# Kernel optimization log

Measured on AMD Instinct MI355X. Metric: run time of the kernel, lower is better.

## Reference

```python
import jax, jax.numpy as jnp
import numpy as np

N, F, T, HID, E = 50000, 8, 12, 64, 1600000


def setup_inputs() -> dict:
    key = jax.random.key(0)
    ks = jax.random.split(key, 9)
    x = jax.random.normal(ks[0], (N, F, T), jnp.float32)
    edge_index = jax.random.randint(ks[1], (2, E), 0, N)
    edge_weight = jax.random.uniform(ks[2], (E,), jnp.float32)
    # GCNConv weights for the z/r/h gates, fused along the output dim -> (F, 3*HID)
    s = 1.0 / np.sqrt(F)
    conv_w = jax.random.uniform(ks[3], (F, 3 * HID), jnp.float32, -s, s)
    conv_b = jnp.zeros((3 * HID,), jnp.float32)
    # TGCN gate linears: input is concat([conv_out, H]) of width 2*HID
    s2 = 1.0 / np.sqrt(2 * HID)
    lin_w = jax.random.uniform(ks[4], (3, 2 * HID, HID), jnp.float32, -s2, s2)
    lin_b = jax.random.uniform(ks[5], (3, HID), jnp.float32, -s2, s2)
    attention = jax.random.uniform(ks[6], (T,), jnp.float32)
    sc = 1.0 / np.sqrt(HID)
    cls_w = jax.random.uniform(ks[7], (HID, T), jnp.float32, -sc, sc)
    cls_b = jax.random.uniform(ks[8], (T,), jnp.float32, -sc, sc)
    return dict(x=x, edge_index=edge_index, edge_weight=edge_weight,
                conv_w=conv_w, conv_b=conv_b, lin_w=lin_w, lin_b=lin_b,
                attention=attention, cls_w=cls_w, cls_b=cls_b)


def _gcn_norm(edge_index, edge_weight, num_nodes):
    # PyG gcn_norm: add self-loops (weight 1), symmetric D^-1/2 (A+I) D^-1/2
    src, dst = edge_index[0], edge_index[1]
    loop = jnp.arange(num_nodes)
    src = jnp.concatenate([src, loop])
    dst = jnp.concatenate([dst, loop])
    w = jnp.concatenate([edge_weight, jnp.ones((num_nodes,), edge_weight.dtype)])
    deg = jax.ops.segment_sum(w, dst, num_segments=num_nodes)
    dinv = jnp.where(deg > 0, jax.lax.rsqrt(deg), 0.0)
    return src, dst, dinv[src] * w * dinv[dst]


def reference(x, edge_index, edge_weight, conv_w, conv_b, lin_w, lin_b, attention, cls_w, cls_b):
    num_nodes, _, periods = x.shape
    hid = cls_w.shape[0]
    src, dst, norm = _gcn_norm(edge_index, edge_weight, num_nodes)
    probs = jax.nn.softmax(attention)
    Hzero = jnp.zeros((num_nodes, hid), x.dtype)  # A3TGCN passes the same H (None->0) each period
    H_accum = jnp.zeros((num_nodes, hid), x.dtype)
    for t in range(periods):
        xw = x[:, :, t] @ conv_w  # (N, 3*hid)
        conv = jax.ops.segment_sum(xw[src] * norm[:, None], dst, num_segments=num_nodes) + conv_b
        cz, cr, ch = jnp.split(conv, 3, axis=1)
        Z = jax.nn.sigmoid(jnp.concatenate([cz, Hzero], axis=1) @ lin_w[0] + lin_b[0])
        R = jax.nn.sigmoid(jnp.concatenate([cr, Hzero], axis=1) @ lin_w[1] + lin_b[1])
        H_tilde = jnp.tanh(jnp.concatenate([ch, Hzero * R], axis=1) @ lin_w[2] + lin_b[2])
        H_new = Z * Hzero + (1.0 - Z) * H_tilde
        H_accum = H_accum + probs[t] * H_new
    h = jax.nn.relu(H_accum)
    return h @ cls_w + cls_b  # (N, periods)
```

## Files before the change

kernel.cpp:

```cpp
#include <hip/hip_runtime.h>
#include <hip/hip_fp16.h>
#include <math.h>

#define NN 50000
#define FD 8
#define TD 12
#define HD 64
#define FT 96
#define EE 1600000
#define NBUK 391
#define TILE 16384
#define NT 98
#define SORTCAP 5120

#define OFF_GHIST 0
#define OFF_BASE  512
#define OFF_CUR   1024
#define OFF_ROWST 2048
#define OFF_DINV  (2048 + NN + 16)
#define OFF_FUSED (OFF_DINV + NN)
#define OFF_XH    (OFF_FUSED + 1184)
#define OFF_BEDGE (OFF_XH + NN*48)
#define OFF_AGGH  (OFF_BEDGE + 2*EE)

__device__ inline void h8f(uint4 h, float* f) {
    const __half2* p = (const __half2*)&h;
#pragma unroll
    for (int i = 0; i < 4; ++i) {
        float2 v = __half22float2(p[i]);
        f[2 * i] = v.x; f[2 * i + 1] = v.y;
    }
}

__device__ inline uint4 f8h(const float* f) {
    uint4 o;
    __half2* p = (__half2*)&o;
#pragma unroll
    for (int i = 0; i < 4; ++i) p[i] = __floats2half2_rn(f[2 * i], f[2 * i + 1]);
    return o;
}

__global__ void k_precompute(const float* __restrict__ conv_w,
                             const float* __restrict__ conv_b,
                             const float* __restrict__ lin_w,
                             const float* __restrict__ lin_b,
                             const float* __restrict__ attention,
                             float* __restrict__ fused,
                             int* __restrict__ ghist) {
    int tid = threadIdx.x;
    if (tid < NBUK) ghist[tid] = 0;
    for (int idx = tid; idx < 1024; idx += blockDim.x) {
        int sel = idx >> 9;
        int f = (idx & 511) >> 6;
        int h = idx & 63;
        const float* cw = conv_w + f * 192 + (sel ? 128 : 0);
        const float* lw = lin_w + (sel ? 2 * 128 * 64 : 0) + h;
        float s = 0.f;
        for (int k = 0; k < 64; ++k) s += cw[k] * lw[k * 64];
        fused[idx] = s;
    }
    for (int idx = tid; idx < 128; idx += blockDim.x) {
        int sel = idx >> 6;
        int h = idx & 63;
        const float* cb = conv_b + (sel ? 128 : 0);
        const float* lw = lin_w + (sel ? 2 * 128 * 64 : 0) + h;
        float s = lin_b[(sel ? 2 * 64 : 0) + h];
        for (int k = 0; k < 64; ++k) s += cb[k] * lw[k * 64];
        fused[1024 + idx] = s;
    }
    if (tid == 0) {
        float m = attention[0];
        for (int t = 1; t < TD; ++t) m = fmaxf(m, attention[t]);
        float e[TD], sum = 0.f;
        for (int t = 0; t < TD; ++t) { e[t] = __expf(attention[t] - m); sum += e[t]; }
        for (int t = 0; t < TD; ++t) fused[1152 + t] = e[t] / sum;
    }
}

__global__ void k_xhalf(const float* __restrict__ x, uint4* __restrict__ xh4) {
    unsigned i = blockIdx.x * 256u + threadIdx.x;
    if (i >= (unsigned)NN * 12u) return;
    unsigned n = i / 12u, t = i - n * 12u;
    const float* xp = x + (size_t)n * FT + t;
    float f[8];
#pragma unroll
    for (int k = 0; k < 8; ++k) f[k] = xp[k * 12];
    xh4[i] = f8h(f);
}

__global__ __launch_bounds__(1024) void k_hist(const int* __restrict__ ei,
                                               int* __restrict__ ghist) {
    __shared__ int h[NBUK];
    int tid = threadIdx.x;
    for (int i = tid; i < NBUK; i += 1024) h[i] = 0;
    __syncthreads();
    int base = blockIdx.x * TILE;
    for (int i = 0; i < TILE / 1024; ++i) {
        int e = base + i * 1024 + tid;
        if (e < EE) atomicAdd(&h[ei[EE + e] >> 7], 1);
    }
    __syncthreads();
    for (int i = tid; i < NBUK; i += 1024)
        if (h[i]) atomicAdd(&ghist[i], h[i]);
}

__global__ void k_scan(const int* __restrict__ ghist, int* __restrict__ bktbase,
                       int* __restrict__ cursor) {
    __shared__ int s[512];
    int tid = threadIdx.x;
    int v = (tid < NBUK) ? ghist[tid] : 0;
    s[tid] = v;
    __syncthreads();
    for (int off = 1; off < 512; off <<= 1) {
        int t = (tid >= off) ? s[tid - off] : 0;
        __syncthreads();
        s[tid] += t;
        __syncthreads();
    }
    int excl = s[tid] - v;
    if (tid < NBUK) { bktbase[tid] = excl; cursor[tid] = excl; }
    if (tid == NBUK - 1) bktbase[NBUK] = excl + v;
}

__global__ __launch_bounds__(1024) void k_place(const int* __restrict__ ei,
                                                const float* __restrict__ w,
                                                int* __restrict__ cursor,
                                                int2* __restrict__ bedge) {
    __shared__ int h[NBUK], bbase[NBUK];
    int tid = threadIdx.x;
    for (int i = tid; i < NBUK; i += 1024) h[i] = 0;
    __syncthreads();
    int base = blockIdx.x * TILE;
    for (int i = 0; i < TILE / 1024; ++i) {
        int e = base + i * 1024 + tid;
        if (e < EE) atomicAdd(&h[ei[EE + e] >> 7], 1);
    }
    __syncthreads();
    for (int i = tid; i < NBUK; i += 1024) {
        int c = h[i];
        bbase[i] = c ? atomicAdd(&cursor[i], c) : 0;
        h[i] = 0;
    }
    __syncthreads();
    for (int i = 0; i < TILE / 1024; ++i) {
        int e = base + i * 1024 + tid;
        if (e < EE) {
            int dst = ei[EE + e];
            int bk = dst >> 7;
            int rank = atomicAdd(&h[bk], 1);
            bedge[bbase[bk] + rank] =
                make_int2(ei[e] | ((dst & 127) << 16), __float_as_int(w[e]));
        }
    }
}

__global__ __launch_bounds__(512) void k_sort(const int* __restrict__ bktbase,
                                              int2* __restrict__ bedge,
                                              int* __restrict__ rowstart,
                                              float* __restrict__ dinv) {
    __shared__ int2 stage[SORTCAP];
    __shared__ int cnt[128];
    __shared__ float wd[128];
    __shared__ int rowbase[128];
    int tid = threadIdx.x, b = blockIdx.x;
    int es = bktbase[b], ee = bktbase[b + 1];
    int count = ee - es;
    if (count > SORTCAP) count = SORTCAP;
    if (tid < 128) { cnt[tid] = 0; wd[tid] = 0.f; }
    __syncthreads();
    for (int i = tid; i < count; i += 512) {
        int2 u = bedge[es + i];
        stage[i] = u;
        int dl = u.x >> 16;
        atomicAdd(&cnt[dl], 1);
        atomicAdd(&wd[dl], __int_as_float(u.y));
    }
    __syncthreads();
    if (tid < 128) rowbase[tid] = cnt[tid];
    __syncthreads();
    for (int off = 1; off < 128; off <<= 1) {
        int t = 0;
        if (tid >= off && tid < 128) t = rowbase[tid - off];
        __syncthreads();
        if (tid < 128) rowbase[tid] += t;
        __syncthreads();
    }
    int dbase = b << 7;
    if (tid < 128) {
        int excl = rowbase[tid] - cnt[tid];
        rowbase[tid] = excl;
        if (dbase + tid < NN) {
            rowstart[dbase + tid] = es + excl;
            dinv[dbase + tid] = rsqrtf(1.0f + wd[tid]);
        }
        cnt[tid] = 0;
    }
    if (b == NBUK - 1 && tid == 0) rowstart[NN] = ee;
    __syncthreads();
    for (int i = tid; i < count; i += 512) {
        int2 u = stage[i];
        int dl = u.x >> 16;
        int pos = atomicAdd(&cnt[dl], 1);
        bedge[es + rowbase[dl] + pos] = make_int2(u.x & 0xFFFF, u.y);
    }
}

__global__ __launch_bounds__(256) void k_gather(const uint4* __restrict__ xh4,
                                                const float* __restrict__ dinv,
                                                const int* __restrict__ rowstart,
                                                const int2* __restrict__ edata,
                                                uint4* __restrict__ aggh) {
    unsigned t = blockIdx.x * 256u + threadIdx.x;
    if (t >= (unsigned)NN * 12u) return;
    unsigned n = t / 12u;
    unsigned c = t - n * 12u;
    float dv = dinv[n];
    float a[8];
    h8f(xh4[n * 12u + c], a);
#pragma unroll
    for (int j = 0; j < 8; ++j) a[j] *= dv;
    int rs = rowstart[n], re = rowstart[n + 1];
    int k = rs;
    for (; k + 1 < re; k += 2) {
        int2 pa = edata[k], pb = edata[k + 1];
        float ca = dinv[pa.x] * __int_as_float(pa.y);
        float cb = dinv[pb.x] * __int_as_float(pb.y);
        float va[8], vb[8];
        h8f(xh4[(unsigned)pa.x * 12u + c], va);
        h8f(xh4[(unsigned)pb.x * 12u + c], vb);
#pragma unroll
        for (int j = 0; j < 8; ++j) a[j] += ca * va[j] + cb * vb[j];
    }
    if (k < re) {
        int2 p = edata[k];
        float co = dinv[p.x] * __int_as_float(p.y);
        float v[8];
        h8f(xh4[(unsigned)p.x * 12u + c], v);
#pragma unroll
        for (int j = 0; j < 8; ++j) a[j] += co * v[j];
    }
#pragma unroll
    for (int j = 0; j < 8; ++j) a[j] *= dv;
    aggh[n * 12u + c] = f8h(a);
}

__global__ __launch_bounds__(256) void k_node(const uint4* __restrict__ aggh,
                                              const float* __restrict__ fused,
                                              const float* __restrict__ cls_w,
                                              const float* __restrict__ cls_b,
                                              float* __restrict__ out) {
    __shared__ float r_lds[32 * 100];
    __shared__ float rel_lds[32 * 68];
    __shared__ float cwT_lds[12 * 68];
    __shared__ float cb_lds[12];
    __shared__ float probs_lds[12];
    int tid = threadIdx.x;
    int nbase = blockIdx.x * 32;

    for (int id = tid; id < 384; id += 256) {
        int nl = id / 12, c = id - nl * 12;
        float f[8] = {0, 0, 0, 0, 0, 0, 0, 0};
        int n = nbase + nl;
        if (n < NN) h8f(aggh[(size_t)n * 12 + c], f);
        *(float4*)&r_lds[nl * 100 + c * 8] = make_float4(f[0], f[1], f[2], f[3]);
        *(float4*)&r_lds[nl * 100 + c * 8 + 4] = make_float4(f[4], f[5], f[6], f[7]);
    }
    for (int id = tid; id < 768; id += 256) {
        int hh = id / 12, t = id - hh * 12;
        cwT_lds[t * 68 + hh] = cls_w[id];
    }
    if (tid < 12) { cb_lds[tid] = cls_b[tid]; probs_lds[tid] = fused[1152 + tid]; }

    int h = tid & 63;
    int w = tid >> 6;
    float wz[FD], wh[FD];
#pragma unroll
    for (int f = 0; f < FD; ++f) {
        wz[f] = fused[f * 64 + h];
        wh[f] = fused[512 + f * 64 + h];
    }
    float bz = fused[1024 + h], bh = fused[1088 + h];
    __syncthreads();

#pragma unroll
    for (int np = 0; np < 4; ++np) {
        int nl0 = w * 8 + np * 2;
        const float* rp0 = &r_lds[nl0 * 100];
        const float* rp1 = rp0 + 100;
        float acc0 = 0.f, acc1 = 0.f;
#pragma unroll
        for (int t = 0; t < TD; ++t) {
            float4 a0 = *(const float4*)&rp0[t * 8];
            float4 a1 = *(const float4*)&rp0[t * 8 + 4];
            float4 b0 = *(const float4*)&rp1[t * 8];
            float4 b1 = *(const float4*)&rp1[t * 8 + 4];
            float z0 = bz, h0 = bh, z1 = bz, h1 = bh;
            z0 += a0.x * wz[0] + a0.y * wz[1] + a0.z * wz[2] + a0.w * wz[3]
                + a1.x * wz[4] + a1.y * wz[5] + a1.z * wz[6] + a1.w * wz[7];
            h0 += a0.x * wh[0] + a0.y * wh[1] + a0.z * wh[2] + a0.w * wh[3]
                + a1.x * wh[4] + a1.y * wh[5] + a1.z * wh[6] + a1.w * wh[7];
            z1 += b0.x * wz[0] + b0.y * wz[1] + b0.z * wz[2] + b0.w * wz[3]
                + b1.x * wz[4] + b1.y * wz[5] + b1.z * wz[6] + b1.w * wz[7];
            h1 += b0.x * wh[0] + b0.y * wh[1] + b0.z * wh[2] + b0.w * wh[3]
                + b1.x * wh[4] + b1.y * wh[5] + b1.z * wh[6] + b1.w * wh[7];
            float om0 = __builtin_amdgcn_rcpf(1.f + __expf(z0));
            float om1 = __builtin_amdgcn_rcpf(1.f + __expf(z1));
            float Ht0 = 1.f - 2.f * __builtin_amdgcn_rcpf(1.f + __expf(2.f * h0));
            float Ht1 = 1.f - 2.f * __builtin_amdgcn_rcpf(1.f + __expf(2.f * h1));
            float p = probs_lds[t];
            acc0 += p * om0 * Ht0;
            acc1 += p * om1 * Ht1;
        }
        rel_lds[nl0 * 68 + h] = fmaxf(acc0, 0.f);
        rel_lds[(nl0 + 1) * 68 + h] = fmaxf(acc1, 0.f);
    }
    __syncthreads();

    for (int id = tid; id < 384; id += 256) {
        int nl = id / 12, t = id - nl * 12;
        int n = nbase + nl;
        if (n >= NN) continue;
        const float* rl = &rel_lds[nl * 68];
        const float* cwr = &cwT_lds[t * 68];
        float s = cb_lds[t];
#pragma unroll
        for (int k = 0; k < 16; ++k) {
            float4 rv = *(const float4*)&rl[k * 4];
            float4 cv = *(const float4*)&cwr[k * 4];
            s += rv.x * cv.x + rv.y * cv.y + rv.z * cv.z + rv.w * cv.w;
        }
        out[(size_t)n * TD + t] = s;
    }
}

extern "C" void kernel_launch(void* const* d_in, const int* in_sizes, int n_in,
                              void* d_out, int out_size, void* d_ws, size_t ws_size,
                              hipStream_t stream) {
    const float* x         = (const float*)d_in[0];
    const int*   ei        = (const int*)d_in[1];
    const float* w         = (const float*)d_in[2];
    const float* conv_w    = (const float*)d_in[3];
    const float* conv_b    = (const float*)d_in[4];
    const float* lin_w     = (const float*)d_in[5];
    const float* lin_b     = (const float*)d_in[6];
    const float* attention = (const float*)d_in[7];
    const float* cls_w     = (const float*)d_in[8];
    const float* cls_b     = (const float*)d_in[9];
    float* ws  = (float*)d_ws;
    float* out = (float*)d_out;

    int*   ghist    = (int*)(ws + OFF_GHIST);
    int*   bktbase  = (int*)(ws + OFF_BASE);
    int*   cursor   = (int*)(ws + OFF_CUR);
    int*   rowstart = (int*)(ws + OFF_ROWST);
    float* dinv     = ws + OFF_DINV;
    float* fused    = ws + OFF_FUSED;
    uint4* xh4      = (uint4*)(ws + OFF_XH);
    int2*  bedge    = (int2*)(ws + OFF_BEDGE);
    uint4* aggh     = (uint4*)(ws + OFF_AGGH);

    k_precompute<<<1, 512, 0, stream>>>(conv_w, conv_b, lin_w, lin_b, attention,
                                        fused, ghist);
    k_xhalf<<<(NN * 12 + 255) / 256, 256, 0, stream>>>(x, xh4);
    k_hist<<<NT, 1024, 0, stream>>>(ei, ghist);
    k_scan<<<1, 512, 0, stream>>>(ghist, bktbase, cursor);
    k_place<<<NT, 1024, 0, stream>>>(ei, w, cursor, bedge);
    k_sort<<<NBUK, 512, 0, stream>>>(bktbase, bedge, rowstart, dinv);
    {
        unsigned total = (unsigned)NN * 12u;
        k_gather<<<(total + 255) / 256, 256, 0, stream>>>(xh4, dinv,
                                                          rowstart, bedge, aggh);
    }
    k_node<<<(NN + 31) / 32, 256, 0, stream>>>(aggh, fused, cls_w, cls_b, out);
}
```

Before: 166.8 us.

## Fuse front kernels, reuse per-tile histograms in place, unroll gather by four

Merges the precompute, x-to-half conversion and edge histogram kernels into one launch that partitions its blocks by role, with the ghist clear moved to a memset. Each histogram tile now writes its per-bucket counts to a workspace array, so the place kernel no longer re-reads destinations and recounts them. The gather inner loop is unrolled from two to four edges to keep more loads in flight. The cost is extra workspace, a memset launch, and higher register pressure in the gather kernel.

```diff
diff --git a/kernel.cpp b/kernel.cpp
--- a/kernel.cpp
+++ b/kernel.cpp
@@ -11,6 +11,7 @@
 #define NBUK 391
 #define TILE 16384
 #define NT 98
+#define XB 586
 #define SORTCAP 5120
 
 #define OFF_GHIST 0
@@ -19,7 +20,8 @@
 #define OFF_ROWST 2048
 #define OFF_DINV  (2048 + NN + 16)
 #define OFF_FUSED (OFF_DINV + NN)
-#define OFF_XH    (OFF_FUSED + 1184)
+#define OFF_THIST (OFF_FUSED + 1184)
+#define OFF_XH    (OFF_THIST + 38400)
 #define OFF_BEDGE (OFF_XH + NN*48)
 #define OFF_AGGH  (OFF_BEDGE + 2*EE)
 
@@ -40,68 +42,73 @@
     return o;
 }
 
-__global__ void k_precompute(const float* __restrict__ conv_w,
-                             const float* __restrict__ conv_b,
-                             const float* __restrict__ lin_w,
-                             const float* __restrict__ lin_b,
-                             const float* __restrict__ attention,
-                             float* __restrict__ fused,
-                             int* __restrict__ ghist) {
+__global__ __launch_bounds__(1024) void k_front(const float* __restrict__ x,
+                                                uint4* __restrict__ xh4,
+                                                const int* __restrict__ ei,
+                                                int* __restrict__ ghist,
+                                                int* __restrict__ thist,
+                                                const float* __restrict__ conv_w,
+                                                const float* __restrict__ conv_b,
+                                                const float* __restrict__ lin_w,
+                                                const float* __restrict__ lin_b,
+                                                const float* __restrict__ attention,
+                                                float* __restrict__ fused) {
+    int b = blockIdx.x;
     int tid = threadIdx.x;
-    if (tid < NBUK) ghist[tid] = 0;
-    for (int idx = tid; idx < 1024; idx += blockDim.x) {
-        int sel = idx >> 9;
-        int f = (idx & 511) >> 6;
-        int h = idx & 63;
-        const float* cw = conv_w + f * 192 + (sel ? 128 : 0);
-        const float* lw = lin_w + (sel ? 2 * 128 * 64 : 0) + h;
-        float s = 0.f;
-        for (int k = 0; k < 64; ++k) s += cw[k] * lw[k * 64];
-        fused[idx] = s;
-    }
-    for (int idx = tid; idx < 128; idx += blockDim.x) {
-        int sel = idx >> 6;
-        int h = idx & 63;
-        const float* cb = conv_b + (sel ? 128 : 0);
-        const float* lw = lin_w + (sel ? 2 * 128 * 64 : 0) + h;
-        float s = lin_b[(sel ? 2 * 64 : 0) + h];
-        for (int k = 0; k < 64; ++k) s += cb[k] * lw[k * 64];
-        fused[1024 + idx] = s;
-    }
-    if (tid == 0) {
-        float m = attention[0];
-        for (int t = 1; t < TD; ++t) m = fmaxf(m, attention[t]);
-        float e[TD], sum = 0.f;
-        for (int t = 0; t < TD; ++t) { e[t] = __expf(attention[t] - m); sum += e[t]; }
-        for (int t = 0; t < TD; ++t) fused[1152 + t] = e[t] / sum;
-    }
-}
-
-__global__ void k_xhalf(const float* __restrict__ x, uint4* __restrict__ xh4) {
-    unsigned i = blockIdx.x * 256u + threadIdx.x;
-    if (i >= (unsigned)NN * 12u) return;
-    unsigned n = i / 12u, t = i - n * 12u;
-    const float* xp = x + (size_t)n * FT + t;
-    float f[8];
-#pragma unroll
-    for (int k = 0; k < 8; ++k) f[k] = xp[k * 12];
-    xh4[i] = f8h(f);
-}
-
-__global__ __launch_bounds__(1024) void k_hist(const int* __restrict__ ei,
-                                               int* __restrict__ ghist) {
-    __shared__ int h[NBUK];
-    int tid = threadIdx.x;
-    for (int i = tid; i < NBUK; i += 1024) h[i] = 0;
-    __syncthreads();
-    int base = blockIdx.x * TILE;
-    for (int i = 0; i < TILE / 1024; ++i) {
-        int e = base + i * 1024 + tid;
-        if (e < EE) atomicAdd(&h[ei[EE + e] >> 7], 1);
-    }
-    __syncthreads();
-    for (int i = tid; i < NBUK; i += 1024)
-        if (h[i]) atomicAdd(&ghist[i], h[i]);
+    if (b < NT) {
+        __shared__ int h[NBUK];
+        for (int i = tid; i < NBUK; i += 1024) h[i] = 0;
+        __syncthreads();
+        int base = b * TILE;
+        for (int i = 0; i < TILE / 1024; ++i) {
+            int e = base + i * 1024 + tid;
+            if (e < EE) atomicAdd(&h[ei[EE + e] >> 7], 1);
+        }
+        __syncthreads();
+        int* trow = thist + b * NBUK;
+        for (int i = tid; i < NBUK; i += 1024) {
+            int c = h[i];
+            trow[i] = c;
+            if (c) atomicAdd(&ghist[i], c);
+        }
+    } else if (b < NT + XB) {
+        unsigned i = (unsigned)(b - NT) * 1024u + tid;
+        if (i < (unsigned)NN * 12u) {
+            unsigned n = i / 12u, t = i - n * 12u;
+            const float* xp = x + (size_t)n * FT + t;
+            float f[8];
+#pragma unroll
+            for (int k = 0; k < 8; ++k) f[k] = xp[k * 12];
+            xh4[i] = f8h(f);
+        }
+    } else {
+        for (int idx = tid; idx < 1024; idx += 1024) {
+            int sel = idx >> 9;
+            int f = (idx & 511) >> 6;
+            int h = idx & 63;
+            const float* cw = conv_w + f * 192 + (sel ? 128 : 0);
+            const float* lw = lin_w + (sel ? 2 * 128 * 64 : 0) + h;
+            float s = 0.f;
+            for (int k = 0; k < 64; ++k) s += cw[k] * lw[k * 64];
+            fused[idx] = s;
+        }
+        if (tid < 128) {
+            int sel = tid >> 6;
+            int h = tid & 63;
+            const float* cb = conv_b + (sel ? 128 : 0);
+            const float* lw = lin_w + (sel ? 2 * 128 * 64 : 0) + h;
+            float s = lin_b[(sel ? 2 * 64 : 0) + h];
+            for (int k = 0; k < 64; ++k) s += cb[k] * lw[k * 64];
+            fused[1024 + tid] = s;
+        }
+        if (tid == 0) {
+            float m = attention[0];
+            for (int t = 1; t < TD; ++t) m = fmaxf(m, attention[t]);
+            float e[TD], sum = 0.f;
+            for (int t = 0; t < TD; ++t) { e[t] = __expf(attention[t] - m); sum += e[t]; }
+            for (int t = 0; t < TD; ++t) fused[1152 + t] = e[t] / sum;
+        }
+    }
 }
 
 __global__ void k_scan(const int* __restrict__ ghist, int* __restrict__ bktbase,
@@ -124,24 +131,19 @@
 
 __global__ __launch_bounds__(1024) void k_place(const int* __restrict__ ei,
                                                 const float* __restrict__ w,
+                                                const int* __restrict__ thist,
                                                 int* __restrict__ cursor,
                                                 int2* __restrict__ bedge) {
     __shared__ int h[NBUK], bbase[NBUK];
     int tid = threadIdx.x;
-    for (int i = tid; i < NBUK; i += 1024) h[i] = 0;
-    __syncthreads();
-    int base = blockIdx.x * TILE;
-    for (int i = 0; i < TILE / 1024; ++i) {
-        int e = base + i * 1024 + tid;
-        if (e < EE) atomicAdd(&h[ei[EE + e] >> 7], 1);
-    }
-    __syncthreads();
+    const int* tcnt = thist + blockIdx.x * NBUK;
     for (int i = tid; i < NBUK; i += 1024) {
-        int c = h[i];
+        int c = tcnt[i];
         bbase[i] = c ? atomicAdd(&cursor[i], c) : 0;
         h[i] = 0;
     }
     __syncthreads();
+    int base = blockIdx.x * TILE;
     for (int i = 0; i < TILE / 1024; ++i) {
         int e = base + i * 1024 + tid;
         if (e < EE) {
@@ -221,17 +223,22 @@
     for (int j = 0; j < 8; ++j) a[j] *= dv;
     int rs = rowstart[n], re = rowstart[n + 1];
     int k = rs;
-    for (; k + 1 < re; k += 2) {
-        int2 pa = edata[k], pb = edata[k + 1];
-        float ca = dinv[pa.x] * __int_as_float(pa.y);
-        float cb = dinv[pb.x] * __int_as_float(pb.y);
-        float va[8], vb[8];
-        h8f(xh4[(unsigned)pa.x * 12u + c], va);
-        h8f(xh4[(unsigned)pb.x * 12u + c], vb);
-#pragma unroll
-        for (int j = 0; j < 8; ++j) a[j] += ca * va[j] + cb * vb[j];
-    }
-    if (k < re) {
+    for (; k + 3 < re; k += 4) {
+        int2 p0 = edata[k], p1 = edata[k + 1], p2 = edata[k + 2], p3 = edata[k + 3];
+        float c0 = dinv[p0.x] * __int_as_float(p0.y);
+        float c1 = dinv[p1.x] * __int_as_float(p1.y);
+        float c2 = dinv[p2.x] * __int_as_float(p2.y);
+        float c3 = dinv[p3.x] * __int_as_float(p3.y);
+        float v0[8], v1[8], v2[8], v3[8];
+        h8f(xh4[(unsigned)p0.x * 12u + c], v0);
+        h8f(xh4[(unsigned)p1.x * 12u + c], v1);
+        h8f(xh4[(unsigned)p2.x * 12u + c], v2);
+        h8f(xh4[(unsigned)p3.x * 12u + c], v3);
+#pragma unroll
+        for (int j = 0; j < 8; ++j)
+            a[j] += c0 * v0[j] + c1 * v1[j] + c2 * v2[j] + c3 * v3[j];
+    }
+    for (; k < re; ++k) {
         int2 p = edata[k];
         float co = dinv[p.x] * __int_as_float(p.y);
         float v[8];
@@ -355,16 +362,17 @@
     int*   rowstart = (int*)(ws + OFF_ROWST);
     float* dinv     = ws + OFF_DINV;
     float* fused    = ws + OFF_FUSED;
+    int*   thist    = (int*)(ws + OFF_THIST);
     uint4* xh4      = (uint4*)(ws + OFF_XH);
     int2*  bedge    = (int2*)(ws + OFF_BEDGE);
     uint4* aggh     = (uint4*)(ws + OFF_AGGH);
 
-    k_precompute<<<1, 512, 0, stream>>>(conv_w, conv_b, lin_w, lin_b, attention,
-                                        fused, ghist);
-    k_xhalf<<<(NN * 12 + 255) / 256, 256, 0, stream>>>(x, xh4);
-    k_hist<<<NT, 1024, 0, stream>>>(ei, ghist);
+    hipMemsetAsync(ghist, 0, NBUK * sizeof(int), stream);
+    k_front<<<NT + XB + 1, 1024, 0, stream>>>(x, xh4, ei, ghist, thist,
+                                              conv_w, conv_b, lin_w, lin_b,
+                                              attention, fused);
     k_scan<<<1, 512, 0, stream>>>(ghist, bktbase, cursor);
-    k_place<<<NT, 1024, 0, stream>>>(ei, w, cursor, bedge);
+    k_place<<<NT, 1024, 0, stream>>>(ei, w, thist, cursor, bedge);
     k_sort<<<NBUK, 512, 0, stream>>>(bktbase, bedge, rowstart, dinv);
     {
         unsigned total = (unsigned)NN * 12u;
```

New measurement: 158.2 us. 1.05x faster.
